# Optimization experiments

Hardware: AMD Instinct MI355X
Metric: run time of the kernel (lower is better)

Reference implementation:

```python
import jax, jax.numpy as jnp
import numpy as np

EPS = 1e-6
HEADS = 8
DIM_HEAD = 64
SCALE = 16.0
DIM = 1024
INNER = HEADS * DIM_HEAD


def _l2norm(t):
    return t / jnp.clip(jnp.linalg.norm(t, axis=-1, keepdims=True), 1e-12)


def setup_inputs() -> dict:
    key = jax.random.key(0)
    k1, k2, k3, k4 = jax.random.split(key, 4)
    b, n = 2, 4096
    x = jax.random.normal(k1, (b, n, DIM), dtype=jnp.float32)
    # weights stored as [in, out] so application is x @ W
    Wq = jax.random.normal(k2, (DIM, INNER), dtype=jnp.float32) * 0.02
    Wkv = jax.random.normal(k3, (DIM, 2 * INNER), dtype=jnp.float32) * 0.02
    Wo = jax.random.normal(k4, (INNER, DIM), dtype=jnp.float32) * 0.02
    return {"x": x, "Wq": Wq, "Wkv": Wkv, "Wo": Wo}


def reference(x, Wq, Wkv, Wo):
    b, n, _ = x.shape
    q = (x @ Wq).reshape(b, n, HEADS, DIM_HEAD).transpose(0, 2, 1, 3)  # b h n d
    kv = x @ Wkv
    k = kv[..., :INNER].reshape(b, n, HEADS, DIM_HEAD).transpose(0, 2, 1, 3)
    v = kv[..., INNER:].reshape(b, n, HEADS, DIM_HEAD).transpose(0, 2, 1, 3)
    q = _l2norm(q)
    k = _l2norm(k)
    # cosine-sim attention: logits = scale * (q.k) - scale, logits <= 0 so exp is stable
    logits = jnp.einsum('bhid,bhjd->bhij', q, k) * SCALE - SCALE
    p = jnp.exp(logits)
    row_sums = jnp.clip(p.sum(axis=-1, keepdims=True), EPS)  # matches per-block EPS clamp in dense case
    out = jnp.einsum('bhij,bhjd->bhid', p, v) / row_sums  # b h n d
    out = out.transpose(0, 2, 1, 3).reshape(b, n, INNER)
    return out @ Wo
```

## Files before the change

kernel.cpp:

```cpp
#include <hip/hip_runtime.h>


typedef _Float16 f16;
typedef _Float16 f16x4 __attribute__((ext_vector_type(4)));
typedef _Float16 f16x8 __attribute__((ext_vector_type(8)));
typedef float f32x4 __attribute__((ext_vector_type(4)));
typedef float f32x16 __attribute__((ext_vector_type(16)));
typedef int i32x4 __attribute__((ext_vector_type(4)));

#define MFMA_F16(a, b, c) __builtin_amdgcn_mfma_f32_16x16x32_f16((a), (b), (c), 0, 0, 0)
#define MFMA32(a, b, c) __builtin_amdgcn_mfma_f32_32x32x16_f16((a), (b), (c), 0, 0, 0)

#define QSCALE 23.083120654223414f
#define EXPBIAS -9.083120654223414f

__device__ __forceinline__ void gl_lds16(const void* g, void* l) {
  __builtin_amdgcn_global_load_lds(
      (const __attribute__((address_space(1))) void*)g,
      (__attribute__((address_space(3))) void*)l, 16, 0, 0);
}

__global__ void transpose_all_kernel(const float* __restrict__ Wq,
                                     const float* __restrict__ Wkv,
                                     const float* __restrict__ Wo,
                                     f16* __restrict__ Wqkv_t, f16* __restrict__ Wo_t) {
  __shared__ float t[64][65];
  const int z = blockIdx.z;
  const float* W; int ldw, col0, K, nc; f16* out;
  if (z == 0)      { W = Wq;  ldw = 512;  col0 = 0;   K = 1024; nc = 8;  out = Wqkv_t; }
  else if (z == 1) { W = Wkv; ldw = 1024; col0 = 0;   K = 1024; nc = 8;  out = Wqkv_t + 512 * 1024; }
  else if (z == 2) { W = Wkv; ldw = 1024; col0 = 512; K = 1024; nc = 8;  out = Wqkv_t + 1024 * 1024; }
  else             { W = Wo;  ldw = 1024; col0 = 0;   K = 512;  nc = 16; out = Wo_t; }
  if ((int)blockIdx.x >= nc || (int)blockIdx.y >= (K >> 6)) return;
  int tx = threadIdx.x, ty = threadIdx.y;
  int c0 = blockIdx.x * 64, k0 = blockIdx.y * 64;
#pragma unroll
  for (int i = 0; i < 8; i++)
    t[ty + i * 8][tx] = W[(long)(k0 + ty + i * 8) * ldw + col0 + c0 + tx];
  __syncthreads();
#pragma unroll
  for (int i = 0; i < 8; i++)
    out[(long)(c0 + ty + i * 8) * K + k0 + tx] = (f16)t[tx][ty + i * 8];
}

__global__ void transpose_v_kernel(const f16* __restrict__ Vb, f16* __restrict__ Vt, int n) {
  __shared__ f16 t[64 * 64];
  const int tid = threadIdx.x;
  const int bh = blockIdx.y;
  const int n0 = blockIdx.x * 64;
  const f16* src = Vb + ((long)bh * n + n0) * 64;
  const int j = tid >> 3, c = tid & 7;
  f16x8 v0 = *(const f16x8*)(src + j * 64 + c * 8);
  f16x8 v1 = *(const f16x8*)(src + (j + 32) * 64 + c * 8);
  *(f16x8*)(&t[j * 64 + ((c ^ (j & 7)) << 3)]) = v0;
  *(f16x8*)(&t[(j + 32) * 64 + ((c ^ (j & 7)) << 3)]) = v1;
  __syncthreads();
  const int d = tid >> 3, cj = tid & 7;
  f16x8 o0, o1;
#pragma unroll
  for (int e = 0; e < 8; e++) {
    int jj = cj * 8 + e;
    o0[e] = t[jj * 64 + (((d >> 3) ^ (jj & 7)) << 3) + (d & 7)];
    o1[e] = t[jj * 64 + ((((d + 32) >> 3) ^ (jj & 7)) << 3) + ((d + 32) & 7)];
  }
  *(f16x8*)(Vt + ((long)bh * 64 + d) * n + n0 + cj * 8) = o0;
  *(f16x8*)(Vt + ((long)bh * 64 + d + 32) * n + n0 + cj * 8) = o1;
}

template <int MODE>
__global__ __launch_bounds__(256, 3)
void gemm_kernel(const f16* __restrict__ A, const f16* __restrict__ Bt,
                 float* __restrict__ C,
                 f16* __restrict__ Qb, f16* __restrict__ Kb, f16* __restrict__ Vb,
                 const float* __restrict__ Axf,
                 int M, int N, int K) {
  __shared__ f16 As[128 * 32];
  __shared__ f16 Bs[128 * 32];
  const int tid = threadIdx.x;
  const int lane = tid & 63;
  const int wid = tid >> 6;
  const int wr = wid >> 1, wc = wid & 1;
  const int lr = lane & 15, lk = lane >> 4;
  const int lin = blockIdx.x;
  const int bx = ((lin & 7) << 3) | ((lin >> 3) & 7);
  const int by = lin >> 6;
  const long m0 = (long)bx * 128;
  const int n0 = by * 128;

  f32x4 acc[4][4] = {};

  const int c0 = tid, c1 = tid + 256;
  const int ar0 = c0 >> 2, ah0 = (c0 & 3) ^ ((ar0 >> 1) & 3);
  const int ar1 = c1 >> 2, ah1 = (c1 & 3) ^ ((ar1 >> 1) & 3);
  const f16* pa0 = A + (m0 + ar0) * K + ah0 * 8;
  const f16* pa1 = A + (m0 + ar1) * K + ah1 * 8;
  const float* pa0f = Axf + (m0 + ar0) * K + ah0 * 8;
  const float* pa1f = Axf + (m0 + ar1) * K + ah1 * 8;
  const f16* pb0 = Bt + (long)(n0 + ar0) * K + ah0 * 8;
  const f16* pb1 = Bt + (long)(n0 + ar1) * K + ah1 * 8;

  float4 a00, a01, a10, a11;
  if (MODE == 1) {
    a00 = *(const float4*)(pa0f);
    a01 = *(const float4*)(pa0f + 4);
    a10 = *(const float4*)(pa1f);
    a11 = *(const float4*)(pa1f + 4);
  }

  for (int k0 = 0; k0 < K; k0 += 32) {
    __syncthreads();
    if (MODE == 1) {
      f16x8 w0, w1;
#pragma unroll
      for (int e = 0; e < 4; e++) {
        w0[e] = (f16)(&a00.x)[e];
        w0[4 + e] = (f16)(&a01.x)[e];
        w1[e] = (f16)(&a10.x)[e];
        w1[4 + e] = (f16)(&a11.x)[e];
      }
      *(f16x8*)(As + c0 * 8) = w0;
      *(f16x8*)(As + c1 * 8) = w1;
    } else {
      gl_lds16(pa0 + k0, As + c0 * 8);
      gl_lds16(pa1 + k0, As + c1 * 8);
    }
    gl_lds16(pb0 + k0, Bs + c0 * 8);
    gl_lds16(pb1 + k0, Bs + c1 * 8);
    __syncthreads();

    if (MODE == 1 && k0 + 32 < K) {
      a00 = *(const float4*)(pa0f + k0 + 32);
      a01 = *(const float4*)(pa0f + k0 + 36);
      a10 = *(const float4*)(pa1f + k0 + 32);
      a11 = *(const float4*)(pa1f + k0 + 36);
    }

    f16x8 af[4], bf[4];
#pragma unroll
    for (int mi = 0; mi < 4; mi++) {
      int row = wr * 64 + mi * 16 + lr;
      int ch = lk ^ ((row >> 1) & 3);
      af[mi] = *(const f16x8*)(As + row * 32 + ch * 8);
    }
#pragma unroll
    for (int ni = 0; ni < 4; ni++) {
      int row = wc * 64 + ni * 16 + lr;
      int ch = lk ^ ((row >> 1) & 3);
      bf[ni] = *(const f16x8*)(Bs + row * 32 + ch * 8);
    }
    __builtin_amdgcn_s_setprio(1);
#pragma unroll
    for (int mi = 0; mi < 4; mi++)
#pragma unroll
      for (int ni = 0; ni < 4; ni++)
        acc[mi][ni] = MFMA_F16(af[mi], bf[ni], acc[mi][ni]);
    __builtin_amdgcn_s_setprio(0);
  }

  if (MODE == 0) {
#pragma unroll
    for (int mi = 0; mi < 4; mi++) {
      long mrow = m0 + wr * 64 + mi * 16 + lk * 4;
#pragma unroll
      for (int r = 0; r < 4; r++)
#pragma unroll
        for (int ni = 0; ni < 4; ni++)
          C[(mrow + r) * N + n0 + wc * 64 + ni * 16 + lr] = acc[mi][ni][r];
    }
  } else {
    const int region = by >> 2;
    const int head = (by & 3) * 2 + wc;
    f16* buf = (region == 0) ? Qb : ((region == 1) ? Kb : Vb);
    const float nscale = (region == 0) ? QSCALE : 1.f;
#pragma unroll
    for (int mi = 0; mi < 4; mi++) {
      float scl[4];
      if (region < 2) {
#pragma unroll
        for (int r = 0; r < 4; r++) {
          float s2 = 0.f;
#pragma unroll
          for (int ni = 0; ni < 4; ni++) s2 += acc[mi][ni][r] * acc[mi][ni][r];
          s2 += __shfl_xor(s2, 1);
          s2 += __shfl_xor(s2, 2);
          s2 += __shfl_xor(s2, 4);
          s2 += __shfl_xor(s2, 8);
          scl[r] = nscale / fmaxf(sqrtf(s2), 1e-12f);
        }
      } else {
#pragma unroll
        for (int r = 0; r < 4; r++) scl[r] = 1.f;
      }
#pragma unroll
      for (int r = 0; r < 4; r++) {
        int m = (int)m0 + wr * 64 + mi * 16 + lk * 4 + r;
        int bb = m >> 12, nn = m & 4095;
        f16* dst = buf + (((long)(bb * 8 + head) * 4096 + nn) << 6);
#pragma unroll
        for (int ni = 0; ni < 4; ni++)
          dst[ni * 16 + lr] = (f16)(acc[mi][ni][r] * scl[r]);
      }
    }
  }
}

__global__ __launch_bounds__(256, 2)
void attn_kernel(const f16* __restrict__ Qb, const f16* __restrict__ Kb,
                 const f16* __restrict__ Vt, f16* __restrict__ Ob, int n) {
  __shared__ f16 Ks[2][128 * 64];
  __shared__ f16 Vs[2][64 * 128];
  const int tid = threadIdx.x, lane = tid & 63, wid = tid >> 6;
  const int ql = lane & 31, hi = lane >> 5;
  const int lin = blockIdx.x;
  const int bh = (lin & 7) | ((lin >> 8) << 3);
  const int qx = (lin >> 3) & 31;
  const long nl = n;
  const f16* Qg = Qb + (long)bh * nl * 64;
  const f16* Kg = Kb + (long)bh * nl * 64;
  const f16* Vg = Vt + (long)bh * 64 * nl;
  const int q0w = qx * 128 + wid * 32;

  f16x8 qf[4];
#pragma unroll
  for (int kc = 0; kc < 4; kc++)
    qf[kc] = *(const f16x8*)(Qg + (long)(q0w + ql) * 64 + kc * 16 + hi * 8);

  int ksrc[4], vsrc[4];
#pragma unroll
  for (int p = 0; p < 4; p++) {
    const int ci = tid + p * 256;
    const int kj = ci >> 3, kc_ = ci & 7;
    ksrc[p] = kj * 64 + ((kc_ ^ (kj & 7)) << 3);
    const int vd = ci >> 4, vc = ci & 15;
    vsrc[p] = vd * n + ((vc ^ (vd & 15)) << 3);
  }

  f32x16 oacc[2][2] = {};
  float rsum0 = 0.f, rsum1 = 0.f;
  f32x16 initv;
#pragma unroll
  for (int e = 0; e < 16; e++) initv[e] = EXPBIAS;
  const auto one2 = __builtin_amdgcn_cvt_pkrtz(1.f, 1.f);

#pragma unroll
  for (int p = 0; p < 4; p++) {
    gl_lds16(Kg + ksrc[p], &Ks[0][(tid + p * 256) * 8]);
    gl_lds16(Vg + vsrc[p], &Vs[0][(tid + p * 256) * 8]);
  }
  __syncthreads();

  const int nt = n >> 7;
  for (int t = 0; t < nt; t++) {
    const int cur = t & 1;
    if (t + 1 < nt) {
      const long kadv = (long)(t + 1) * 8192;
      const long vadv = (long)(t + 1) * 128;
#pragma unroll
      for (int p = 0; p < 4; p++) {
        gl_lds16(Kg + kadv + ksrc[p], &Ks[cur ^ 1][(tid + p * 256) * 8]);
        gl_lds16(Vg + vadv + vsrc[p], &Vs[cur ^ 1][(tid + p * 256) * 8]);
      }
    }

    f32x16 s_cur, s_nxt;
    {
      const int j = ql, sw = j & 7;
      __builtin_amdgcn_s_setprio(1);
      const f16x8 k0 = *(const f16x8*)(&Ks[cur][j * 64 + ((hi ^ sw) << 3)]);
      s_cur = MFMA32(k0, qf[0], initv);
#pragma unroll
      for (int kc = 1; kc < 4; kc++) {
        const f16x8 kf = *(const f16x8*)(&Ks[cur][j * 64 + ((((kc << 1) | hi) ^ sw) << 3)]);
        s_cur = MFMA32(kf, qf[kc], s_cur);
      }
      __builtin_amdgcn_s_setprio(0);
    }

#pragma unroll
    for (int jt = 0; jt < 4; jt++) {
      if (jt < 3) {
        const int j = (jt + 1) * 32 + ql, sw = j & 7;
        const f16x8 k0 = *(const f16x8*)(&Ks[cur][j * 64 + ((hi ^ sw) << 3)]);
        s_nxt = MFMA32(k0, qf[0], initv);
#pragma unroll
        for (int kc = 1; kc < 4; kc++) {
          const f16x8 kf = *(const f16x8*)(&Ks[cur][j * 64 + ((((kc << 1) | hi) ^ sw) << 3)]);
          s_nxt = MFMA32(kf, qf[kc], s_nxt);
        }
      }

      int w[8];
#pragma unroll
      for (int m = 0; m < 8; m++) {
        const float pa = __builtin_amdgcn_exp2f(s_cur[2 * m]);
        const float pb = __builtin_amdgcn_exp2f(s_cur[2 * m + 1]);
        const auto h = __builtin_amdgcn_cvt_pkrtz(pa, pb);
        if (m & 1)
          rsum1 = __builtin_amdgcn_fdot2(h, one2, rsum1, false);
        else
          rsum0 = __builtin_amdgcn_fdot2(h, one2, rsum0, false);
        w[m] = __builtin_bit_cast(int, h);
      }
#pragma unroll
      for (int kl = 0; kl < 2; kl++) {
        int a0 = w[4 * kl + 0], a1 = w[4 * kl + 1];
        int a2 = w[4 * kl + 2], a3 = w[4 * kl + 3];
        asm volatile("v_permlane32_swap_b32 %0, %1" : "+v"(a0), "+v"(a2));
        asm volatile("v_permlane32_swap_b32 %0, %1" : "+v"(a1), "+v"(a3));
        i32x4 fi = {a0, a1, a2, a3};
        const f16x8 pfrag = __builtin_bit_cast(f16x8, fi);
        const int kb = jt * 2 + kl;
        __builtin_amdgcn_s_setprio(1);
#pragma unroll
        for (int dt = 0; dt < 2; dt++) {
          const int d = dt * 32 + ql;
          const f16x8 vf =
              *(const f16x8*)(&Vs[cur][d * 128 + ((((kb << 1) | hi) ^ (d & 15)) << 3)]);
          oacc[kl][dt] = MFMA32(pfrag, vf, oacc[kl][dt]);
        }
        __builtin_amdgcn_s_setprio(0);
      }
      if (jt < 3) s_cur = s_nxt;
    }

    __syncthreads();
  }

  float rsum = rsum0 + rsum1;
  rsum += __shfl_xor(rsum, 32);
  const int bb = bh >> 3, hh = bh & 7;
#pragma unroll
  for (int r = 0; r < 16; r++) {
    const int qloc = (r & 3) + 8 * (r >> 2) + 4 * hi;
    const float sm = __shfl(rsum, qloc);
    const float inv = 1.f / fmaxf(sm, 0.016384f);
    f16* dst = Ob + (((long)(bb * 4096 + q0w + qloc)) << 9) + hh * 64;
    dst[ql] = (f16)((oacc[0][0][r] + oacc[1][0][r]) * inv);
    dst[32 + ql] = (f16)((oacc[0][1][r] + oacc[1][1][r]) * inv);
  }
}

extern "C" void kernel_launch(void* const* d_in, const int* in_sizes, int n_in,
                              void* d_out, int out_size, void* d_ws, size_t ws_size,
                              hipStream_t stream) {
  const float* x   = (const float*)d_in[0];
  const float* Wq  = (const float*)d_in[1];
  const float* Wkv = (const float*)d_in[2];
  const float* Wo  = (const float*)d_in[3];
  float* out = (float*)d_out;

  char* ws = (char*)d_ws;
  f16* Vt     = (f16*)(ws);
  f16* Wqkv_t = (f16*)(ws + 16777216);
  f16* Wo_t   = (f16*)(ws + 19922944);
  f16* Qb     = (f16*)(ws + 20971520);
  f16* Kb     = (f16*)(ws + 29360128);
  f16* Vb     = (f16*)(ws + 37748736);
  f16* At     = (f16*)(ws + 46137344);

  transpose_all_kernel<<<dim3(16, 16, 4), dim3(64, 8), 0, stream>>>(Wq, Wkv, Wo, Wqkv_t, Wo_t);

  gemm_kernel<1><<<768, 256, 0, stream>>>(nullptr, Wqkv_t, nullptr, Qb, Kb, Vb, x,
                                          8192, 1536, 1024);
  transpose_v_kernel<<<dim3(64, 16), 256, 0, stream>>>(Vb, Vt, 4096);
  attn_kernel<<<512, 256, 0, stream>>>(Qb, Kb, Vt, At, 4096);
  gemm_kernel<0><<<512, 256, 0, stream>>>(At, Wo_t, out, nullptr, nullptr, nullptr, nullptr,
                                          8192, 1024, 512);
}
```

Measured before the change: 151.0 us.

## Load K tiles directly into registers instead of staging through LDS

The K tile is no longer staged in LDS. Each wave loads its K fragments straight from global memory into registers (16 f16x8 per lane) and prefetches the next tile's fragments right after each QK MFMA group. This removes the K LDS traffic and halves shared memory use. In exchange it raises register pressure, drops the software pipelining of S computation across jt, and makes every wave fetch K redundantly from global or L2.

```diff
diff --git a/kernel.cpp b/kernel.cpp
--- a/kernel.cpp
+++ b/kernel.cpp
@@ -207,7 +207,6 @@
 __global__ __launch_bounds__(256, 2)
 void attn_kernel(const f16* __restrict__ Qb, const f16* __restrict__ Kb,
                  const f16* __restrict__ Vt, f16* __restrict__ Ob, int n) {
-  __shared__ f16 Ks[2][128 * 64];
   __shared__ f16 Vs[2][64 * 128];
   const int tid = threadIdx.x, lane = tid & 63, wid = tid >> 6;
   const int ql = lane & 31, hi = lane >> 5;
@@ -225,15 +224,21 @@
   for (int kc = 0; kc < 4; kc++)
     qf[kc] = *(const f16x8*)(Qg + (long)(q0w + ql) * 64 + kc * 16 + hi * 8);
 
-  int ksrc[4], vsrc[4];
+  int vsrc[4];
 #pragma unroll
   for (int p = 0; p < 4; p++) {
     const int ci = tid + p * 256;
-    const int kj = ci >> 3, kc_ = ci & 7;
-    ksrc[p] = kj * 64 + ((kc_ ^ (kj & 7)) << 3);
     const int vd = ci >> 4, vc = ci & 15;
     vsrc[p] = vd * n + ((vc ^ (vd & 15)) << 3);
   }
+
+  const f16* Kw = Kg + (long)ql * 64 + hi * 8;
+  f16x8 kreg[4][4];
+#pragma unroll
+  for (int jt = 0; jt < 4; jt++)
+#pragma unroll
+    for (int kc = 0; kc < 4; kc++)
+      kreg[jt][kc] = *(const f16x8*)(Kw + (jt * 32) * 64 + kc * 16);
 
   f32x16 oacc[2][2] = {};
   float rsum0 = 0.f, rsum1 = 0.f;
@@ -243,57 +248,39 @@
   const auto one2 = __builtin_amdgcn_cvt_pkrtz(1.f, 1.f);
 
 #pragma unroll
-  for (int p = 0; p < 4; p++) {
-    gl_lds16(Kg + ksrc[p], &Ks[0][(tid + p * 256) * 8]);
+  for (int p = 0; p < 4; p++)
     gl_lds16(Vg + vsrc[p], &Vs[0][(tid + p * 256) * 8]);
-  }
   __syncthreads();
 
   const int nt = n >> 7;
   for (int t = 0; t < nt; t++) {
     const int cur = t & 1;
     if (t + 1 < nt) {
-      const long kadv = (long)(t + 1) * 8192;
-      const long vadv = (long)(t + 1) * 128;
-#pragma unroll
-      for (int p = 0; p < 4; p++) {
-        gl_lds16(Kg + kadv + ksrc[p], &Ks[cur ^ 1][(tid + p * 256) * 8]);
+      const long vadv = (long)(t + 1) << 7;
+#pragma unroll
+      for (int p = 0; p < 4; p++)
         gl_lds16(Vg + vadv + vsrc[p], &Vs[cur ^ 1][(tid + p * 256) * 8]);
-      }
-    }
-
-    f32x16 s_cur, s_nxt;
-    {
-      const int j = ql, sw = j & 7;
+    }
+    const long knext = ((long)((t + 1) & (nt - 1)) << 7) * 64;
+
+#pragma unroll
+    for (int jt = 0; jt < 4; jt++) {
       __builtin_amdgcn_s_setprio(1);
-      const f16x8 k0 = *(const f16x8*)(&Ks[cur][j * 64 + ((hi ^ sw) << 3)]);
-      s_cur = MFMA32(k0, qf[0], initv);
-#pragma unroll
-      for (int kc = 1; kc < 4; kc++) {
-        const f16x8 kf = *(const f16x8*)(&Ks[cur][j * 64 + ((((kc << 1) | hi) ^ sw) << 3)]);
-        s_cur = MFMA32(kf, qf[kc], s_cur);
-      }
+      f32x16 s = MFMA32(kreg[jt][0], qf[0], initv);
+      s = MFMA32(kreg[jt][1], qf[1], s);
+      s = MFMA32(kreg[jt][2], qf[2], s);
+      s = MFMA32(kreg[jt][3], qf[3], s);
       __builtin_amdgcn_s_setprio(0);
-    }
-
-#pragma unroll
-    for (int jt = 0; jt < 4; jt++) {
-      if (jt < 3) {
-        const int j = (jt + 1) * 32 + ql, sw = j & 7;
-        const f16x8 k0 = *(const f16x8*)(&Ks[cur][j * 64 + ((hi ^ sw) << 3)]);
-        s_nxt = MFMA32(k0, qf[0], initv);
-#pragma unroll
-        for (int kc = 1; kc < 4; kc++) {
-          const f16x8 kf = *(const f16x8*)(&Ks[cur][j * 64 + ((((kc << 1) | hi) ^ sw) << 3)]);
-          s_nxt = MFMA32(kf, qf[kc], s_nxt);
-        }
-      }
+
+#pragma unroll
+      for (int kc = 0; kc < 4; kc++)
+        kreg[jt][kc] = *(const f16x8*)(Kw + knext + (jt * 32) * 64 + kc * 16);
 
       int w[8];
 #pragma unroll
       for (int m = 0; m < 8; m++) {
-        const float pa = __builtin_amdgcn_exp2f(s_cur[2 * m]);
-        const float pb = __builtin_amdgcn_exp2f(s_cur[2 * m + 1]);
+        const float pa = __builtin_amdgcn_exp2f(s[2 * m]);
+        const float pb = __builtin_amdgcn_exp2f(s[2 * m + 1]);
         const auto h = __builtin_amdgcn_cvt_pkrtz(pa, pb);
         if (m & 1)
           rsum1 = __builtin_amdgcn_fdot2(h, one2, rsum1, false);
@@ -320,7 +307,6 @@
         }
         __builtin_amdgcn_s_setprio(0);
       }
-      if (jt < 3) s_cur = s_nxt;
     }
 
     __syncthreads();
```

Measured after the change: 198.9 us. 31.8% more time.
